# Optimization experiments

Hardware: AMD Instinct MI355X
Metric: run time of the kernel (lower is better)

## Reference

```python
import jax, jax.numpy as jnp
import numpy as np

MAX_SPAN_WIDTH = 30


def setup_inputs() -> dict:
    key = jax.random.key(0)
    ks = jax.random.split(key, 10)
    num_words, D = 1024, 768          # BERT-base hidden size
    num_spans = 8192                  # candidate spans
    feat, ffnn = 20, 1000             # feature_size, ffnn_size
    span_dim = 3 * D + feat           # 2324

    mention_doc = jax.random.normal(ks[0], (num_words, D), jnp.float32)
    starts = jax.random.randint(ks[1], (num_spans,), 0, num_words, jnp.int32)
    widths = jax.random.randint(ks[2], (num_spans,), 1, MAX_SPAN_WIDTH + 1, jnp.int32)
    ends = jnp.minimum(starts + widths - 1, num_words - 1).astype(jnp.int32)

    def lin(k, fan_in, shape):
        return (jax.random.normal(k, shape, jnp.float32) / np.sqrt(fan_in)).astype(jnp.float32)

    return {
        "mention_doc": mention_doc,
        "w_width_emb": jax.random.normal(ks[3], (MAX_SPAN_WIDTH, feat), jnp.float32) * 0.02,
        "w_head": lin(ks[4], D, (D,)),
        "b_head": jnp.zeros((), jnp.float32),
        "W1": lin(ks[5], span_dim, (span_dim, ffnn)),
        "b1": jnp.zeros((ffnn,), jnp.float32),
        "W2": lin(ks[6], ffnn, (ffnn, ffnn)),
        "b2": jnp.zeros((ffnn,), jnp.float32),
        "W3": lin(ks[7], ffnn, (ffnn, 1)),
        "b3": jnp.zeros((1,), jnp.float32),
        "candidate_starts": starts,
        "candidate_ends": ends,
        "top_span_num": 409,  # min(3900, int(1024 * 0.4))
    }


def _span_scores(mention_doc, w_width_emb, w_head, b_head, W1, b1, W2, b2, W3, b3,
                 starts, ends):
    num_words = mention_doc.shape[0]
    start_emb = mention_doc[starts]                       # [S, D]
    end_emb = mention_doc[ends]                           # [S, D]
    span_widths = ends - starts + 1
    width_emb = w_width_emb[span_widths - 1]              # [S, F]
    # span word indices, clamped (same as torch.clamp(..., max=num_words-1))
    idxes = jnp.minimum(jnp.arange(MAX_SPAN_WIDTH, dtype=starts.dtype)[None, :]
                        + starts[:, None], num_words - 1)  # [S, W]
    head_scores = mention_doc @ w_head + b_head            # [num_words]
    hs = head_scores[idxes]                                # [S, W]
    mask = jnp.arange(MAX_SPAN_WIDTH)[None, :] < span_widths[:, None]
    hs = jnp.where(mask, hs, -jnp.inf)
    attn = jax.nn.softmax(hs, axis=1)                      # [S, W]
    attended = jnp.einsum("sw,swd->sd", attn, mention_doc[idxes])  # [S, D]
    span_emb = jnp.concatenate([start_emb, end_emb, width_emb, attended], axis=-1)
    h = jax.nn.relu(span_emb @ W1 + b1)
    h = jax.nn.relu(h @ W2 + b2)
    return (h @ W3 + b3)[:, 0]                             # [S]


def _extract_top_spans(scores, starts, ends, top_span_num, num_words):
    """Greedy sorted selection with crossing-span (NMS-style) suppression."""
    order = jnp.argsort(-scores)                           # descending by score
    pos = jnp.arange(num_words)

    def step(carry, span_idx):
        max_end, min_start, count, selected = carry
        s = starts[span_idx]
        e = ends[span_idx]
        dup = e == max_end[s]                              # same (start, max-end) already chosen
        cross1 = jnp.any((pos > s) & (pos <= e) & (max_end > e))
        cross2 = jnp.any((pos >= s) & (pos < e) & (min_start < s))
        accept = (count < top_span_num) & ~dup & ~cross1 & ~cross2
        max_end = max_end.at[s].max(jnp.where(accept, e, -1))
        min_start = min_start.at[e].min(jnp.where(accept, s, num_words))
        w = jnp.minimum(count, top_span_num - 1)
        selected = selected.at[w].set(
            jnp.where(accept, span_idx.astype(jnp.int32), selected[w]))
        return (max_end, min_start, count + accept.astype(jnp.int32), selected), None

    init = (jnp.full((num_words,), -1, jnp.int32),
            jnp.full((num_words,), num_words, jnp.int32),
            jnp.int32(0),
            jnp.full((top_span_num,), -1, jnp.int32))
    (_, _, _, selected), _ = jax.lax.scan(step, init, order.astype(jnp.int32))

    # final sort by (start, end); unfilled (-1) slots sort to the back
    big = num_words * num_words
    keys = jnp.where(selected >= 0,
                     starts[selected] * num_words + ends[selected], big)
    return selected[jnp.argsort(keys)]                     # [top_span_num], -1 padded


def reference(mention_doc, w_width_emb, w_head, b_head, W1, b1, W2, b2, W3, b3,
              candidate_starts, candidate_ends, top_span_num):
    scores = _span_scores(mention_doc, w_width_emb, w_head, b_head,
                          W1, b1, W2, b2, W3, b3,
                          candidate_starts, candidate_ends)
    top_idxes = _extract_top_spans(scores, candidate_starts, candidate_ends,
                                   int(top_span_num), mention_doc.shape[0])
    return scores, top_idxes
```

## Files before the change

kernel.cpp:

```cpp
#include <hip/hip_runtime.h>
#include <hip/hip_bf16.h>
#include <stdint.h>

#define NW   1024
#define D    768
#define NS   8192
#define MAXW 30
#define FFNN 1000
#define FEAT 20

typedef __attribute__((ext_vector_type(8))) short bf16x8;
typedef __attribute__((ext_vector_type(4))) float f32x4;
#define MFMA16 __builtin_amdgcn_mfma_f32_16x16x32_bf16

#define O_P    0
#define O_P4   3072000
#define O_HS   3102000
#define O_ATT  3103024
#define O_PS   3365168
#define O_H1R  3504432

__device__ inline ushort f2b(float v) {
    __hip_bfloat16 b = __float2bfloat16(v);
    return *(ushort*)&b;
}
__device__ inline float b2f(ushort u) {
    __hip_bfloat16 b = *(__hip_bfloat16*)&u;
    return __bfloat162float(b);
}

__global__ __launch_bounds__(256) void k_head(const float* __restrict__ doc,
                                              const float* __restrict__ wh,
                                              const float* __restrict__ bh,
                                              float* __restrict__ hs) {
    int wid = threadIdx.x >> 6, lane = threadIdx.x & 63;
    int word = blockIdx.x * 4 + wid;
    const float* row = doc + word * D;
    float acc = 0.f;
    for (int d = lane; d < D; d += 64) acc += row[d] * wh[d];
    #pragma unroll
    for (int o = 32; o; o >>= 1) acc += __shfl_down(acc, o);
    if (lane == 0) hs[word] = acc + bh[0];
}

__global__ __launch_bounds__(256) void k_p4(const float* __restrict__ wwe,
                                            const float* __restrict__ W1,
                                            float* __restrict__ P4) {
    int o = blockIdx.x * 256 + threadIdx.x;
    if (o >= 30 * FFNN) return;
    int wi = o / FFNN, j = o - wi * FFNN;
    float acc = 0.f;
    #pragma unroll
    for (int f = 0; f < FEAT; ++f) acc += wwe[wi * FEAT + f] * W1[(1536 + f) * FFNN + j];
    P4[o] = acc;
}

__global__ __launch_bounds__(256) void k_split(const float* __restrict__ src,
                                               ushort* __restrict__ h,
                                               ushort* __restrict__ l, int n) {
    int i = blockIdx.x * 256 + threadIdx.x;
    if (i >= n) return;
    float v = src[i];
    ushort hi = f2b(v);
    float r = v - b2f(hi);
    h[i] = hi;
    l[i] = f2b(r);
}

__global__ void k_tw1(const float* __restrict__ W1,
                      ushort* __restrict__ TH, ushort* __restrict__ TL) {
    __shared__ float tile[32][33];
    int tx = threadIdx.x, ty = threadIdx.y;
    int k0 = blockIdx.x * 32, n0 = blockIdx.y * 32, z = blockIdx.z;
    int roff = (z == 0) ? 0 : (z == 1) ? 768 : 1556;
    #pragma unroll
    for (int i = 0; i < 4; ++i) {
        int kk = ty + i * 8;
        float v = (n0 + tx < FFNN) ? W1[(size_t)(roff + k0 + kk) * FFNN + n0 + tx] : 0.f;
        tile[kk][tx] = v;
    }
    __syncthreads();
    #pragma unroll
    for (int i = 0; i < 4; ++i) {
        int nn = ty + i * 8;
        float v = tile[tx][nn];
        ushort hi = f2b(v);
        float r = v - b2f(hi);
        size_t o = (size_t)z * 1024 * D + (size_t)(n0 + nn) * D + k0 + tx;
        TH[o] = hi;
        TL[o] = f2b(r);
    }
}

__global__ void k_tw2(const float* __restrict__ W2,
                      ushort* __restrict__ TH, ushort* __restrict__ TL) {
    __shared__ float tile[32][33];
    int tx = threadIdx.x, ty = threadIdx.y;
    int k0 = blockIdx.x * 32, n0 = blockIdx.y * 32;
    #pragma unroll
    for (int i = 0; i < 4; ++i) {
        int kk = ty + i * 8;
        float v = (k0 + kk < FFNN && n0 + tx < FFNN)
                    ? W2[(size_t)(k0 + kk) * FFNN + n0 + tx] : 0.f;
        tile[kk][tx] = v;
    }
    __syncthreads();
    #pragma unroll
    for (int i = 0; i < 4; ++i) {
        int nn = ty + i * 8;
        int k = k0 + tx;
        float v = tile[tx][nn];
        ushort hi = f2b(v);
        float r = v - b2f(hi);
        size_t o = (size_t)(n0 + nn) * 1024 + k;
        TH[o] = hi;
        TL[o] = f2b(r);
    }
}

__global__ __launch_bounds__(256) void k_gemmPm(const ushort* __restrict__ Ah_g,
                                                const ushort* __restrict__ Al_g,
                                                const ushort* __restrict__ Bh_g,
                                                const ushort* __restrict__ Bl_g,
                                                float* __restrict__ Pout) {
    __shared__ ushort LDS[2][12288];
    int tid = threadIdx.x;
    int orig = blockIdx.x;
    int t = (orig & 7) * 48 + (orig >> 3);
    int pair = t >> 4, colt = t & 15;
    int z = pair >> 3, rowt = pair & 7;
    int row0 = rowt * 128, col0 = colt * 64;
    size_t zoff = (size_t)z * 1024 * D;
    const ushort* Bh_z = Bh_g + zoff;
    const ushort* Bl_z = Bl_g + zoff;
    float* C = Pout + (size_t)z * NW * FFNN;
    int w = tid >> 6, l = tid & 63;
    int wr = w >> 1, wc = w & 1;
    int fr = l & 15, kb = l >> 4;
    int rA = tid >> 2, p = tid & 3;
    int q = p ^ ((rA >> 1) & 3);
    f32x4 acc[4][2] = {};
    int cur = 0;
    #define STAGE_P(d, kt)                                                                  \
        do {                                                                                \
            int kg = (kt) + q * 8;                                                          \
            __builtin_amdgcn_global_load_lds((const uint*)(Ah_g + (size_t)(row0 + rA) * D + kg),      (uint*)&LDS[d][(0 * 256 + tid) * 8], 16, 0, 0); \
            __builtin_amdgcn_global_load_lds((const uint*)(Ah_g + (size_t)(row0 + rA + 64) * D + kg), (uint*)&LDS[d][(1 * 256 + tid) * 8], 16, 0, 0); \
            __builtin_amdgcn_global_load_lds((const uint*)(Al_g + (size_t)(row0 + rA) * D + kg),      (uint*)&LDS[d][(2 * 256 + tid) * 8], 16, 0, 0); \
            __builtin_amdgcn_global_load_lds((const uint*)(Al_g + (size_t)(row0 + rA + 64) * D + kg), (uint*)&LDS[d][(3 * 256 + tid) * 8], 16, 0, 0); \
            __builtin_amdgcn_global_load_lds((const uint*)(Bh_z + (size_t)(col0 + rA) * D + kg),      (uint*)&LDS[d][(4 * 256 + tid) * 8], 16, 0, 0); \
            __builtin_amdgcn_global_load_lds((const uint*)(Bl_z + (size_t)(col0 + rA) * D + kg),      (uint*)&LDS[d][(5 * 256 + tid) * 8], 16, 0, 0); \
        } while (0)
    STAGE_P(0, 0);
    __syncthreads();
    for (int kt = 0; kt < D; kt += 32) {
        if (kt + 32 < D) STAGE_P(cur ^ 1, kt + 32);
        bf16x8 af[4], alf[4], bfr[2], blf[2];
        #pragma unroll
        for (int mt = 0; mt < 4; ++mt) {
            int r = wr * 64 + mt * 16 + fr;
            int sl = (kb ^ ((r >> 1) & 3)) * 8;
            af[mt]  = *(const bf16x8*)&LDS[cur][r * 32 + sl];
            alf[mt] = *(const bf16x8*)&LDS[cur][4096 + r * 32 + sl];
        }
        #pragma unroll
        for (int nt = 0; nt < 2; ++nt) {
            int c = wc * 32 + nt * 16 + fr;
            int sl = (kb ^ ((c >> 1) & 3)) * 8;
            bfr[nt] = *(const bf16x8*)&LDS[cur][8192 + c * 32 + sl];
            blf[nt] = *(const bf16x8*)&LDS[cur][10240 + c * 32 + sl];
        }
        #pragma unroll
        for (int mt = 0; mt < 4; ++mt)
            #pragma unroll
            for (int nt = 0; nt < 2; ++nt) {
                acc[mt][nt] = MFMA16(af[mt], bfr[nt], acc[mt][nt], 0, 0, 0);
                acc[mt][nt] = MFMA16(af[mt], blf[nt], acc[mt][nt], 0, 0, 0);
                acc[mt][nt] = MFMA16(alf[mt], bfr[nt], acc[mt][nt], 0, 0, 0);
            }
        __syncthreads();
        cur ^= 1;
    }
    #pragma unroll
    for (int mt = 0; mt < 4; ++mt)
        #pragma unroll
        for (int nt = 0; nt < 2; ++nt)
            #pragma unroll
            for (int r = 0; r < 4; ++r) {
                int row = row0 + wr * 64 + mt * 16 + kb * 4 + r;
                int col = col0 + wc * 32 + nt * 16 + fr;
                if (col < FFNN) C[(size_t)row * FFNN + col] = acc[mt][nt][r];
            }
}

__global__ __launch_bounds__(256) void k_gemm2m(const ushort* __restrict__ Ah_g,
                                                const ushort* __restrict__ Al_g,
                                                const ushort* __restrict__ Bh_g,
                                                const ushort* __restrict__ Bl_g,
                                                const float* __restrict__ b2,
                                                const float* __restrict__ W3,
                                                float* __restrict__ PS) {
    __shared__ ushort LDS[2][4][128 * 32];
    int tid = threadIdx.x;
    int orig = blockIdx.x;
    int xcd = orig & 7, idx = orig >> 3;
    int rowt = xcd * 8 + (idx & 7), colt = idx >> 3;
    int row0 = rowt * 128, col0 = colt * 128;
    int w = tid >> 6, l = tid & 63;
    int wr = w >> 1, wc = w & 1;
    int fr = l & 15, kb = l >> 4;
    int r0 = tid >> 2, p = tid & 3;
    int r1 = r0 + 64;
    int q0 = p ^ ((r0 >> 1) & 3);
    int q1 = p ^ ((r1 >> 1) & 3);
    int base0 = (w * 64) * 8;
    int base1 = (256 + w * 64) * 8;
    f32x4 acc[4][4] = {};
    int cur = 0;
    #define STAGE_2(d, kt)                                                                  \
        do {                                                                                \
            int kg0 = (kt) + q0 * 8, kg1 = (kt) + q1 * 8;                                   \
            __builtin_amdgcn_global_load_lds((const uint*)(Ah_g + (size_t)(row0 + r0) * 1000 + kg0), (uint*)&LDS[d][0][base0], 16, 0, 0); \
            __builtin_amdgcn_global_load_lds((const uint*)(Al_g + (size_t)(row0 + r0) * 1000 + kg0), (uint*)&LDS[d][1][base0], 16, 0, 0); \
            __builtin_amdgcn_global_load_lds((const uint*)(Bh_g + (size_t)(col0 + r0) * 1024 + kg0), (uint*)&LDS[d][2][base0], 16, 0, 0); \
            __builtin_amdgcn_global_load_lds((const uint*)(Bl_g + (size_t)(col0 + r0) * 1024 + kg0), (uint*)&LDS[d][3][base0], 16, 0, 0); \
            __builtin_amdgcn_global_load_lds((const uint*)(Ah_g + (size_t)(row0 + r1) * 1000 + kg1), (uint*)&LDS[d][0][base1], 16, 0, 0); \
            __builtin_amdgcn_global_load_lds((const uint*)(Al_g + (size_t)(row0 + r1) * 1000 + kg1), (uint*)&LDS[d][1][base1], 16, 0, 0); \
            __builtin_amdgcn_global_load_lds((const uint*)(Bh_g + (size_t)(col0 + r1) * 1024 + kg1), (uint*)&LDS[d][2][base1], 16, 0, 0); \
            __builtin_amdgcn_global_load_lds((const uint*)(Bl_g + (size_t)(col0 + r1) * 1024 + kg1), (uint*)&LDS[d][3][base1], 16, 0, 0); \
        } while (0)
    STAGE_2(0, 0);
    __syncthreads();
    for (int kt = 0; kt < 1024; kt += 32) {
        if (kt + 32 < 1024) STAGE_2(cur ^ 1, kt + 32);
        bf16x8 af[4], alf[4], bfr[4], blf[4];
        #pragma unroll
        for (int mt = 0; mt < 4; ++mt) {
            int r = wr * 64 + mt * 16 + fr;
            int sl = (kb ^ ((r >> 1) & 3)) * 8;
            af[mt]  = *(const bf16x8*)&LDS[cur][0][r * 32 + sl];
            alf[mt] = *(const bf16x8*)&LDS[cur][1][r * 32 + sl];
        }
        #pragma unroll
        for (int nt = 0; nt < 4; ++nt) {
            int c = wc * 64 + nt * 16 + fr;
            int sl = (kb ^ ((c >> 1) & 3)) * 8;
            bfr[nt] = *(const bf16x8*)&LDS[cur][2][c * 32 + sl];
            blf[nt] = *(const bf16x8*)&LDS[cur][3][c * 32 + sl];
        }
        #pragma unroll
        for (int mt = 0; mt < 4; ++mt)
            #pragma unroll
            for (int nt = 0; nt < 4; ++nt) {
                acc[mt][nt] = MFMA16(af[mt], bfr[nt], acc[mt][nt], 0, 0, 0);
                acc[mt][nt] = MFMA16(af[mt], blf[nt], acc[mt][nt], 0, 0, 0);
                acc[mt][nt] = MFMA16(alf[mt], bfr[nt], acc[mt][nt], 0, 0, 0);
            }
        __syncthreads();
        cur ^= 1;
    }
    float w3v[4], b2v[4];
    #pragma unroll
    for (int nt = 0; nt < 4; ++nt) {
        int col = col0 + wc * 64 + nt * 16 + fr;
        bool cv = col < FFNN;
        w3v[nt] = cv ? W3[col] : 0.f;
        b2v[nt] = cv ? b2[col] : 0.f;
    }
    #pragma unroll
    for (int mt = 0; mt < 4; ++mt) {
        #pragma unroll
        for (int r = 0; r < 4; ++r) {
            float pp = 0.f;
            #pragma unroll
            for (int nt = 0; nt < 4; ++nt) {
                float v = fmaxf(acc[mt][nt][r] + b2v[nt], 0.f);
                pp = fmaf(v, w3v[nt], pp);
            }
            pp += __shfl_xor(pp, 1);
            pp += __shfl_xor(pp, 2);
            pp += __shfl_xor(pp, 4);
            pp += __shfl_xor(pp, 8);
            if (fr == 0) {
                int row = row0 + wr * 64 + mt * 16 + kb * 4 + r;
                PS[row * 16 + colt * 2 + wc] = pp;
            }
        }
    }
}

__global__ __launch_bounds__(256) void k_h1(const float* __restrict__ P,
                                            const float* __restrict__ P4,
                                            const float* __restrict__ hs,
                                            const float* __restrict__ b1,
                                            const int* __restrict__ starts,
                                            const int* __restrict__ ends,
                                            ushort* __restrict__ H1h,
                                            ushort* __restrict__ H1l) {
    __shared__ float shs[32];
    int s = blockIdx.x;
    int tid = threadIdx.x;
    int st = starts[s], en = ends[s];
    int width = en - st + 1;
    if (tid < MAXW) {
        int idx = st + tid; if (idx > NW - 1) idx = NW - 1;
        shs[tid] = hs[idx];
    }
    __syncthreads();
    float v[MAXW];
    float mx = -3.0e38f;
    #pragma unroll
    for (int w = 0; w < MAXW; ++w) {
        float x = shs[w];
        v[w] = (w < width) ? x : -3.0e38f;
        mx = fmaxf(mx, v[w]);
    }
    float sum = 0.f;
    #pragma unroll
    for (int w = 0; w < MAXW; ++w) { v[w] = expf(v[w] - mx); sum += v[w]; }
    float inv = 1.f / sum;
    if (tid >= 250) return;
    const float4* P1r = (const float4*)(P + (size_t)st * FFNN);
    const float4* P2r = (const float4*)(P + (size_t)NW * FFNN + (size_t)en * FFNN);
    const float*  P3  = P + 2 * (size_t)NW * FFNN;
    const float4* P4r = (const float4*)(P4 + (size_t)(width - 1) * FFNN);
    const float4* b1v = (const float4*)b1;
    float4 a = P1r[tid], b = P2r[tid], c = P4r[tid], d = b1v[tid];
    float4 acc = {a.x + b.x + c.x + d.x,
                  a.y + b.y + c.y + d.y,
                  a.z + b.z + c.z + d.z,
                  a.w + b.w + c.w + d.w};
    for (int w = 0; w < width; ++w) {
        float aw = v[w] * inv;
        float4 p3 = ((const float4*)(P3 + (size_t)(st + w) * FFNN))[tid];
        acc.x = fmaf(aw, p3.x, acc.x);
        acc.y = fmaf(aw, p3.y, acc.y);
        acc.z = fmaf(aw, p3.z, acc.z);
        acc.w = fmaf(aw, p3.w, acc.w);
    }
    float rv[4] = {fmaxf(acc.x, 0.f), fmaxf(acc.y, 0.f), fmaxf(acc.z, 0.f), fmaxf(acc.w, 0.f)};
    ushort4 hi, lo;
    ushort* hp = (ushort*)&hi;
    ushort* lp = (ushort*)&lo;
    #pragma unroll
    for (int j = 0; j < 4; ++j) {
        ushort h = f2b(rv[j]);
        float r = rv[j] - b2f(h);
        hp[j] = h;
        lp[j] = f2b(r);
    }
    *(ushort4*)(H1h + (size_t)s * FFNN + tid * 4) = hi;
    *(ushort4*)(H1l + (size_t)s * FFNN + tid * 4) = lo;
}

__global__ __launch_bounds__(256) void k_score2(const float* __restrict__ PS,
                                                const float* __restrict__ b3,
                                                float* __restrict__ out) {
    int r = blockIdx.x * 256 + threadIdx.x;
    if (r >= NS) return;
    float s = 0.f;
    #pragma unroll
    for (int b = 0; b < 16; ++b) s += PS[r * 16 + b];
    out[r] = s + b3[0];
}

__global__ __launch_bounds__(256) void k_rankA(const float* __restrict__ scores,
                                               int* __restrict__ RANK) {
    __shared__ unsigned long long tile[256];
    int i = blockIdx.x * 256 + threadIdx.x;
    int j = blockIdx.y * 256 + threadIdx.x;
    unsigned uj = __float_as_uint(scores[j]);
    unsigned mj = (uj >> 31) ? ~uj : (uj | 0x80000000u);
    tile[threadIdx.x] = ((unsigned long long)(~mj) << 32) | (unsigned)j;
    __syncthreads();
    unsigned u = __float_as_uint(scores[i]);
    unsigned m = (u >> 31) ? ~u : (u | 0x80000000u);
    unsigned long long key = ((unsigned long long)(~m) << 32) | (unsigned)i;
    int r = 0;
    #pragma unroll 8
    for (int q = 0; q < 256; ++q) r += (tile[q] < key);
    if (r) atomicAdd(&RANK[i], r);
}

__global__ __launch_bounds__(256) void k_rankB(const int* __restrict__ RANK,
                                               const int* __restrict__ starts,
                                               const int* __restrict__ ends,
                                               unsigned long long* __restrict__ pk) {
    int i = blockIdx.x * 256 + threadIdx.x;
    pk[RANK[i]] = ((unsigned long long)(unsigned)i << 32) |
                  ((unsigned)starts[i] << 16) | (unsigned)ends[i];
}

__global__ __launch_bounds__(64) void k_masks(const unsigned long long* __restrict__ pk,
                                              unsigned long long* __restrict__ MC,
                                              unsigned long long* __restrict__ ME,
                                              unsigned long long* __restrict__ MG) {
    int lane = threadIdx.x;
    int c = blockIdx.x;
    unsigned long long p = pk[c * 64 + lane];
    int s = (int)((p >> 16) & 0xFFFF);
    int e = (int)(p & 0xFFFF);
    unsigned long long conf = 0, eqm = 0, gtm = 0;
    for (int r = 1; r < 64; ++r) {
        int j = (lane + r) & 63;
        int sj = __shfl(s, j);
        int ej = __shfl(e, j);
        unsigned long long bit = 1ull << j;
        bool cross = ((sj > s) & (sj <= e) & (ej > e)) |
                     ((ej >= s) & (ej < e) & (sj < s));
        if (cross) conf |= bit;
        if (sj == s) { if (ej == e) eqm |= bit; else if (ej > e) gtm |= bit; }
    }
    MC[c * 64 + lane] = conf;
    ME[c * 64 + lane] = eqm;
    MG[c * 64 + lane] = gtm;
}

__global__ __launch_bounds__(64) void k_scan(const unsigned long long* __restrict__ pk,
                                             const unsigned long long* __restrict__ MC,
                                             const unsigned long long* __restrict__ ME,
                                             const unsigned long long* __restrict__ MG,
                                             int top, int* __restrict__ SEL,
                                             int* __restrict__ SELKEY,
                                             int* __restrict__ CNT) {
    __shared__ int mxs[NW];
    __shared__ int mne[NW];
    __shared__ int mxe[NW];
    int lane = threadIdx.x;
    unsigned long long lower = (1ull << lane) - 1ull;
    for (int p = lane; p < NW; p += 64) { mxs[p] = -1; mne[p] = NW; mxe[p] = -1; }
    __syncthreads();
    int count = 0;
    unsigned long long pc = pk[lane];
    unsigned long long conf = MC[lane], eqm = ME[lane], gtm = MG[lane];
    for (int c = 0; c < NS / 64 && count < top; ++c) {
        unsigned long long pn = 0, cn = 0, en2 = 0, gn = 0;
        if (c + 1 < NS / 64) {
            int o = (c + 1) * 64 + lane;
            pn = pk[o]; cn = MC[o]; en2 = ME[o]; gn = MG[o];
        }
        int span = (int)(pc >> 32);
        int s = (int)((pc >> 16) & 0xFFFF);
        int e = (int)(pc & 0xFFFF);
        int bad = (mxs[e] > s) | (mne[s] < e);
        int g = mxe[s];
        bool gdup = (g == e), ggt = (g > e);
        unsigned long long pending = __ballot(!bad), committed = 0;
        unsigned long long relv = (conf | eqm | gtm) & lower;
        while (pending) {
            bool mine = (pending >> lane) & 1;
            bool ready = mine && ((pending & relv) == 0ull);
            unsigned long long cb = committed & lower;
            bool rej = (cb & conf) != 0ull;
            bool gt_any = ggt || ((cb & gtm) != 0ull);
            bool eq_any = gdup || ((cb & eqm) != 0ull);
            bool acc_now = ready && !rej && !(eq_any && !gt_any);
            committed |= __ballot(acc_now);
            pending &= ~__ballot(ready);
        }
        int allowed = top - count;
        while (__popcll(committed) > allowed)
            committed &= ~(1ull << (63 - __builtin_clzll(committed)));
        if ((committed >> lane) & 1) {
            int pos = count + __popcll(committed & lower);
            SEL[pos] = span;
            SELKEY[pos] = s * NW + e;
            atomicMax(&mxe[s], e);
            #pragma unroll
            for (int k = 0; k < MAXW - 1; ++k) {
                if (k < e - s) {
                    atomicMax(&mxs[s + k], s);
                    atomicMin(&mne[s + 1 + k], e);
                }
            }
        }
        count += __popcll(committed);
        __syncthreads();
        pc = pn; conf = cn; eqm = en2; gtm = gn;
    }
    if (lane == 0) *CNT = count;
}

__global__ __launch_bounds__(512) void k_sort(const int* __restrict__ SEL,
                                              const int* __restrict__ SELKEY,
                                              const int* __restrict__ CNT,
                                              int top, float* __restrict__ out_idx) {
    __shared__ int keys[512];
    __shared__ int vals[512];
    int cnt = *CNT;
    int r = threadIdx.x;
    if (r < top) {
        keys[r] = (r < cnt) ? SELKEY[r] : NW * NW;
        vals[r] = (r < cnt) ? SEL[r] : -1;
    }
    __syncthreads();
    if (r < top) {
        int kr = keys[r];
        int rank = 0;
        for (int q = 0; q < top; ++q) {
            int kq = keys[q];
            rank += (kq < kr) || (kq == kr && q < r);
        }
        out_idx[rank] = (float)vals[r];
    }
}

extern "C" void kernel_launch(void* const* d_in, const int* in_sizes, int n_in,
                              void* d_out, int out_size, void* d_ws, size_t ws_size,
                              hipStream_t stream) {
    const float* doc = (const float*)d_in[0];
    const float* wwe = (const float*)d_in[1];
    const float* wh  = (const float*)d_in[2];
    const float* bh  = (const float*)d_in[3];
    const float* W1  = (const float*)d_in[4];
    const float* b1  = (const float*)d_in[5];
    const float* W2  = (const float*)d_in[6];
    const float* b2  = (const float*)d_in[7];
    const float* W3  = (const float*)d_in[8];
    const float* b3  = (const float*)d_in[9];
    const int* starts = (const int*)d_in[10];
    const int* ends   = (const int*)d_in[11];
    int top = out_size - NS;

    float* ws  = (float*)d_ws;
    float* P   = ws + O_P;
    float* P4  = ws + O_P4;
    float* HS  = ws + O_HS;
    float* PS  = ws + O_PS;
    float* H1R = ws + O_H1R;
    ushort* H1H = (ushort*)H1R;
    ushort* H1L = (ushort*)(H1R + 4096000);
    ushort* W1TH = (ushort*)H1R;
    ushort* W1TL = (ushort*)(H1R + 1179648);
    ushort* DOCH = (ushort*)(H1R + 2359296);
    ushort* DOCL = (ushort*)(H1R + 2752512);
    ushort* W2TH = (ushort*)ws;
    ushort* W2TL = (ushort*)(ws + 524288);
    unsigned long long* PK = (unsigned long long*)H1R;
    int* SEL    = (int*)(ws + O_ATT);
    int* SELKEY = SEL + 512;
    int* CNT    = SEL + 1024;
    int* RANK   = SEL + 2048;
    unsigned long long* MC = (unsigned long long*)(ws + O_PS);
    unsigned long long* ME = MC + NS;
    unsigned long long* MG = MC + 2 * NS;
    float* outs = (float*)d_out;

    k_head<<<NW / 4, 256, 0, stream>>>(doc, wh, bh, HS);
    k_p4<<<(30 * FFNN + 255) / 256, 256, 0, stream>>>(wwe, W1, P4);

    k_split<<<(NW * D + 255) / 256, 256, 0, stream>>>(doc, DOCH, DOCL, NW * D);
    {
        dim3 g(24, 32, 3), b(32, 8);
        k_tw1<<<g, b, 0, stream>>>(W1, W1TH, W1TL);
    }
    k_gemmPm<<<384, 256, 0, stream>>>(DOCH, DOCL, W1TH, W1TL, P);

    k_h1<<<NS, 256, 0, stream>>>(P, P4, HS, b1, starts, ends, H1H, H1L);

    {
        dim3 g(32, 32), b(32, 8);
        k_tw2<<<g, b, 0, stream>>>(W2, W2TH, W2TL);
    }
    k_gemm2m<<<512, 256, 0, stream>>>(H1H, H1L, W2TH, W2TL, b2, W3, PS);

    k_score2<<<NS / 256, 256, 0, stream>>>(PS, b3, outs);

    hipMemsetAsync(RANK, 0, NS * sizeof(int), stream);
    {
        dim3 g(NS / 256, NS / 256);
        k_rankA<<<g, 256, 0, stream>>>(outs, RANK);
    }
    k_rankB<<<NS / 256, 256, 0, stream>>>(RANK, starts, ends, PK);
    k_masks<<<NS / 64, 64, 0, stream>>>(PK, MC, ME, MG);
    k_scan<<<1, 64, 0, stream>>>(PK, MC, ME, MG, top, SEL, SELKEY, CNT);
    k_sort<<<1, 512, 0, stream>>>(SEL, SELKEY, CNT, top, outs + NS);
}
```

Measured before the change: 231.3 us.

## Sort spans by start for cache locality in h1 and fuse preprocessing kernels

```diff
diff --git a/kernel.cpp b/kernel.cpp
--- a/kernel.cpp
+++ b/kernel.cpp
@@ -29,42 +29,42 @@
     return __bfloat162float(b);
 }
 
-__global__ __launch_bounds__(256) void k_head(const float* __restrict__ doc,
-                                              const float* __restrict__ wh,
-                                              const float* __restrict__ bh,
-                                              float* __restrict__ hs) {
-    int wid = threadIdx.x >> 6, lane = threadIdx.x & 63;
-    int word = blockIdx.x * 4 + wid;
-    const float* row = doc + word * D;
-    float acc = 0.f;
-    for (int d = lane; d < D; d += 64) acc += row[d] * wh[d];
-    #pragma unroll
-    for (int o = 32; o; o >>= 1) acc += __shfl_down(acc, o);
-    if (lane == 0) hs[word] = acc + bh[0];
-}
-
-__global__ __launch_bounds__(256) void k_p4(const float* __restrict__ wwe,
-                                            const float* __restrict__ W1,
-                                            float* __restrict__ P4) {
-    int o = blockIdx.x * 256 + threadIdx.x;
-    if (o >= 30 * FFNN) return;
-    int wi = o / FFNN, j = o - wi * FFNN;
-    float acc = 0.f;
-    #pragma unroll
-    for (int f = 0; f < FEAT; ++f) acc += wwe[wi * FEAT + f] * W1[(1536 + f) * FFNN + j];
-    P4[o] = acc;
-}
-
-__global__ __launch_bounds__(256) void k_split(const float* __restrict__ src,
-                                               ushort* __restrict__ h,
-                                               ushort* __restrict__ l, int n) {
-    int i = blockIdx.x * 256 + threadIdx.x;
-    if (i >= n) return;
-    float v = src[i];
-    ushort hi = f2b(v);
-    float r = v - b2f(hi);
-    h[i] = hi;
-    l[i] = f2b(r);
+__global__ __launch_bounds__(256) void k_pre(const float* __restrict__ doc,
+                                             const float* __restrict__ wh,
+                                             const float* __restrict__ bh,
+                                             float* __restrict__ hs,
+                                             const float* __restrict__ wwe,
+                                             const float* __restrict__ W1,
+                                             float* __restrict__ P4,
+                                             ushort* __restrict__ DOCH,
+                                             ushort* __restrict__ DOCL) {
+    int b = blockIdx.x;
+    if (b < 256) {
+        int wid = threadIdx.x >> 6, lane = threadIdx.x & 63;
+        int word = b * 4 + wid;
+        const float* row = doc + word * D;
+        float acc = 0.f;
+        for (int d = lane; d < D; d += 64) acc += row[d] * wh[d];
+        #pragma unroll
+        for (int o = 32; o; o >>= 1) acc += __shfl_down(acc, o);
+        if (lane == 0) hs[word] = acc + bh[0];
+    } else if (b < 256 + 118) {
+        int o = (b - 256) * 256 + threadIdx.x;
+        if (o >= 30 * FFNN) return;
+        int wi = o / FFNN, j = o - wi * FFNN;
+        float acc = 0.f;
+        #pragma unroll
+        for (int f = 0; f < FEAT; ++f) acc += wwe[wi * FEAT + f] * W1[(1536 + f) * FFNN + j];
+        P4[o] = acc;
+    } else {
+        int i = (b - 374) * 256 + threadIdx.x;
+        if (i >= NW * D) return;
+        float v = doc[i];
+        ushort hi = f2b(v);
+        float r = v - b2f(hi);
+        DOCH[i] = hi;
+        DOCL[i] = f2b(r);
+    }
 }
 
 __global__ void k_tw1(const float* __restrict__ W1,
@@ -116,6 +116,31 @@
         TH[o] = hi;
         TL[o] = f2b(r);
     }
+}
+
+__global__ __launch_bounds__(256) void k_permA(const int* __restrict__ starts,
+                                               int* __restrict__ PRANK) {
+    __shared__ int ts[256];
+    int i = blockIdx.x * 256 + threadIdx.x;
+    int j = blockIdx.y * 256 + threadIdx.x;
+    ts[threadIdx.x] = starts[j];
+    __syncthreads();
+    int si = starts[i];
+    int jbase = blockIdx.y * 256;
+    int r = 0;
+    #pragma unroll 8
+    for (int q = 0; q < 256; ++q) {
+        int sj = ts[q];
+        int jj = jbase + q;
+        r += (sj < si) || ((sj == si) & (jj < i));
+    }
+    if (r) atomicAdd(&PRANK[i], r);
+}
+
+__global__ __launch_bounds__(256) void k_permB(const int* __restrict__ PRANK,
+                                               int* __restrict__ PERM) {
+    int i = blockIdx.x * 256 + threadIdx.x;
+    PERM[PRANK[i]] = i;
 }
 
 __global__ __launch_bounds__(256) void k_gemmPm(const ushort* __restrict__ Ah_g,
@@ -295,12 +320,15 @@
                                             const float* __restrict__ b1,
                                             const int* __restrict__ starts,
                                             const int* __restrict__ ends,
+                                            const int* __restrict__ PERM,
                                             ushort* __restrict__ H1h,
                                             ushort* __restrict__ H1l) {
     __shared__ float shs[32];
-    int s = blockIdx.x;
+    int bid = blockIdx.x;
+    int i = ((bid & 7) << 10) | (bid >> 3);
     int tid = threadIdx.x;
-    int st = starts[s], en = ends[s];
+    int span = PERM[i];
+    int st = starts[span], en = ends[span];
     int width = en - st + 1;
     if (tid < MAXW) {
         int idx = st + tid; if (idx > NW - 1) idx = NW - 1;
@@ -349,19 +377,20 @@
         hp[j] = h;
         lp[j] = f2b(r);
     }
-    *(ushort4*)(H1h + (size_t)s * FFNN + tid * 4) = hi;
-    *(ushort4*)(H1l + (size_t)s * FFNN + tid * 4) = lo;
+    *(ushort4*)(H1h + (size_t)i * FFNN + tid * 4) = hi;
+    *(ushort4*)(H1l + (size_t)i * FFNN + tid * 4) = lo;
 }
 
 __global__ __launch_bounds__(256) void k_score2(const float* __restrict__ PS,
                                                 const float* __restrict__ b3,
+                                                const int* __restrict__ PERM,
                                                 float* __restrict__ out) {
     int r = blockIdx.x * 256 + threadIdx.x;
     if (r >= NS) return;
     float s = 0.f;
     #pragma unroll
     for (int b = 0; b < 16; ++b) s += PS[r * 16 + b];
-    out[r] = s + b3[0];
+    out[PERM[r]] = s + b3[0];
 }
 
 __global__ __launch_bounds__(256) void k_rankA(const float* __restrict__ scores,
@@ -540,23 +569,30 @@
     int* SEL    = (int*)(ws + O_ATT);
     int* SELKEY = SEL + 512;
     int* CNT    = SEL + 1024;
-    int* RANK   = SEL + 2048;
+    int* PRANK  = SEL + 2048;
+    int* RANK   = SEL + 2048 + 8192;
+    int* PERM   = SEL + 2048 + 16384;
     unsigned long long* MC = (unsigned long long*)(ws + O_PS);
     unsigned long long* ME = MC + NS;
     unsigned long long* MG = MC + 2 * NS;
     float* outs = (float*)d_out;
 
-    k_head<<<NW / 4, 256, 0, stream>>>(doc, wh, bh, HS);
-    k_p4<<<(30 * FFNN + 255) / 256, 256, 0, stream>>>(wwe, W1, P4);
-
-    k_split<<<(NW * D + 255) / 256, 256, 0, stream>>>(doc, DOCH, DOCL, NW * D);
+    hipMemsetAsync(PRANK, 0, 2 * NS * sizeof(int), stream);
+
+    k_pre<<<3446, 256, 0, stream>>>(doc, wh, bh, HS, wwe, W1, P4, DOCH, DOCL);
     {
         dim3 g(24, 32, 3), b(32, 8);
         k_tw1<<<g, b, 0, stream>>>(W1, W1TH, W1TL);
     }
+    {
+        dim3 g(NS / 256, NS / 256);
+        k_permA<<<g, 256, 0, stream>>>(starts, PRANK);
+    }
+    k_permB<<<NS / 256, 256, 0, stream>>>(PRANK, PERM);
+
     k_gemmPm<<<384, 256, 0, stream>>>(DOCH, DOCL, W1TH, W1TL, P);
 
-    k_h1<<<NS, 256, 0, stream>>>(P, P4, HS, b1, starts, ends, H1H, H1L);
+    k_h1<<<NS, 256, 0, stream>>>(P, P4, HS, b1, starts, ends, PERM, H1H, H1L);
 
     {
         dim3 g(32, 32), b(32, 8);
@@ -564,9 +600,8 @@
     }
     k_gemm2m<<<512, 256, 0, stream>>>(H1H, H1L, W2TH, W2TL, b2, W3, PS);
 
-    k_score2<<<NS / 256, 256, 0, stream>>>(PS, b3, outs);
-
-    hipMemsetAsync(RANK, 0, NS * sizeof(int), stream);
+    k_score2<<<NS / 256, 256, 0, stream>>>(PS, b3, PERM, outs);
+
     {
         dim3 g(NS / 256, NS / 256);
         k_rankA<<<g, 256, 0, stream>>>(outs, RANK);
```

Result: slower. 238.6 us (+3.1%).
